# Optimization experiments

Hardware: AMD Instinct MI355X
Metric: run time of the kernel (lower is better)

## Reference

```python
import jax, jax.numpy as jnp
import numpy as np

D = 1024
H = 16
DH = D // H
DFF = 4096
EPS = 1e-5


def new_gelu(u):
    # HF NewGELUActivation: 0.5*u*(1+tanh(sqrt(2/pi)*(u+0.044715*u^3)))
    c = np.sqrt(2.0 / np.pi).astype(np.float32)
    return 0.5 * u * (1.0 + jnp.tanh(c * (u + 0.044715 * u ** 3)))


def layer_norm(u, g, b):
    mu = jnp.mean(u, axis=-1, keepdims=True)
    var = jnp.mean((u - mu) ** 2, axis=-1, keepdims=True)
    return (u - mu) * jax.lax.rsqrt(var + EPS) * g + b


def setup_inputs() -> dict:
    key = jax.random.key(0)
    ks = jax.random.split(key, 12)
    s = 0.02
    inp = {
        "x": jax.random.normal(ks[0], (4, 1024, D), dtype=jnp.float32),
        "Wq": jax.random.normal(ks[1], (D, D), dtype=jnp.float32) * s,
        "bq": jnp.zeros((D,), jnp.float32),
        "Wk": jax.random.normal(ks[2], (D, D), dtype=jnp.float32) * s,
        "bk": jnp.zeros((D,), jnp.float32),
        "Wv": jax.random.normal(ks[3], (D, D), dtype=jnp.float32) * s,
        "bv": jnp.zeros((D,), jnp.float32),
        "Wo": jax.random.normal(ks[4], (D, D), dtype=jnp.float32) * s,
        "bo": jnp.zeros((D,), jnp.float32),
        "g1": jnp.ones((D,), jnp.float32),
        "b1": jnp.zeros((D,), jnp.float32),
        "W1": jax.random.normal(ks[5], (D, DFF), dtype=jnp.float32) * s,
        "bm1": jnp.zeros((DFF,), jnp.float32),
        "W2": jax.random.normal(ks[6], (DFF, D), dtype=jnp.float32) * s,
        "bm2": jnp.zeros((D,), jnp.float32),
        "g2": jnp.ones((D,), jnp.float32),
        "b2": jnp.zeros((D,), jnp.float32),
    }
    return inp


def reference(x, Wq, bq, Wk, bk, Wv, bv, Wo, bo, g1, b1, W1, bm1, W2, bm2, g2, b2):
    B, S, _ = x.shape
    q = (x @ Wq + bq).reshape(B, S, H, DH)
    k = (x @ Wk + bk).reshape(B, S, H, DH)
    v = (x @ Wv + bv).reshape(B, S, H, DH)
    scores = jnp.einsum("bshd,bthd->bhst", q, k) / np.sqrt(DH).astype(np.float32)
    probs = jax.nn.softmax(scores, axis=-1)
    attn = jnp.einsum("bhst,bthd->bshd", probs, v).reshape(B, S, D)
    attn = attn @ Wo + bo
    x1 = layer_norm(x + attn, g1, b1)
    mlp = new_gelu(x1 @ W1 + bm1) @ W2 + bm2
    out = layer_norm(x1 + mlp, g2, b2)
    return out
```

## Files before the change

kernel.cpp:

```cpp
#include <hip/hip_runtime.h>

#define D_    1024
#define HH    16
#define DHEAD 64
#define DFF_  4096
#define NTOK  4096
#define SQLEN 1024

typedef unsigned short ushort_t;
typedef __attribute__((ext_vector_type(8))) short short8;
typedef __attribute__((ext_vector_type(4))) float floatx4;

#define LOG2E 1.44269504f

__device__ __forceinline__ unsigned short f2bf(float f) {
  union { float f; unsigned u; } x; x.f = f;
  unsigned r = x.u + 0x7fffu + ((x.u >> 16) & 1u);
  return (unsigned short)(r >> 16);
}
__device__ __forceinline__ float bf2f(unsigned short u) {
  union { unsigned u; float f; } x; x.u = ((unsigned)u) << 16;
  return x.f;
}
__device__ __forceinline__ unsigned pack2bf_fast(float a, float b) {
  union { float f; unsigned u; } x, y; x.f = a; y.f = b;
  return __builtin_amdgcn_perm(y.u + 0x8000u, x.u + 0x8000u, 0x07060302u);
}
__device__ __forceinline__ float fast_exp2(float x) {
  return __builtin_amdgcn_exp2f(x);
}
__device__ __forceinline__ float fast_gelu(float u) {
  float u2 = u * u;
  float arg = u * (2.30220414f + 0.10294307f * u2);
  float e = __builtin_amdgcn_exp2f(arg);
  float r = __builtin_amdgcn_rcpf(e + 1.0f);
  return u - u * r;
}

__device__ __forceinline__ void async_ld16(const void* g, void* l) {
  __builtin_amdgcn_global_load_lds(
      (const __attribute__((address_space(1))) unsigned int*)g,
      (__attribute__((address_space(3))) unsigned int*)l, 16, 0, 0);
}

__global__ __launch_bounds__(256) void prep_kernel(
    const float* __restrict__ x, const float* __restrict__ Wq,
    const float* __restrict__ Wk, const float* __restrict__ Wv,
    const float* __restrict__ Wo, const float* __restrict__ W1,
    const float* __restrict__ W2,
    ushort_t* __restrict__ xb, ushort_t* __restrict__ wqkvt,
    ushort_t* __restrict__ wot, ushort_t* __restrict__ w1t,
    ushort_t* __restrict__ w2t) {
  int bid = blockIdx.x, tid = threadIdx.x;
  if (bid < 4096) {
    int i = bid * 256 + tid;
    float4 v = ((const float4*)x)[i];
    ushort4 o;
    o.x = f2bf(v.x); o.y = f2bf(v.y); o.z = f2bf(v.z); o.w = f2bf(v.w);
    ((ushort4*)xb)[i] = o;
    return;
  }
  __shared__ float tile[32][33];
  const float* W; ushort_t* T; int K, N, n0, k0;
  if (bid < 8192) {
    int id = bid - 4096, z = id >> 10, xy = id & 1023;
    W = (z == 0) ? Wq : (z == 1) ? Wk : (z == 2) ? Wv : Wo;
    T = (z < 3) ? wqkvt + (size_t)z * D_ * D_ : wot;
    K = D_; N = D_;
    n0 = (xy & 31) * 32; k0 = (xy >> 5) * 32;
  } else if (bid < 12288) {
    int id = bid - 8192;
    W = W1; T = w1t; K = D_; N = DFF_;
    n0 = (id & 127) * 32; k0 = (id >> 7) * 32;
  } else {
    int id = bid - 12288;
    W = W2; T = w2t; K = DFF_; N = D_;
    n0 = (id & 31) * 32; k0 = (id >> 5) * 32;
  }
  int tx = tid & 31, ty = tid >> 5;
#pragma unroll
  for (int i = 0; i < 4; i++)
    tile[ty + i * 8][tx] = W[(size_t)(k0 + ty + i * 8) * N + n0 + tx];
  __syncthreads();
#pragma unroll
  for (int i = 0; i < 4; i++)
    T[(size_t)(n0 + ty + i * 8) * K + k0 + tx] = f2bf(tile[tx][ty + i * 8]);
}

template <int MODE>
__global__ __launch_bounds__(256) void gemm_bf16(
    const ushort_t* __restrict__ A, const ushort_t* __restrict__ Bt,
    int M, int N, int K, int Ks, int nb,
    const float* __restrict__ bias0, const float* __restrict__ bias1,
    const float* __restrict__ bias2,
    ushort_t* __restrict__ o0, ushort_t* __restrict__ o1, ushort_t* __restrict__ o2) {
  __shared__ alignas(16) ushort_t sA[2][128 * 32];
  __shared__ alignas(16) ushort_t sB[2][128 * 32];
  int tid = threadIdx.x;
  int w = tid >> 6, lane = tid & 63, quad = lane >> 4, l16 = lane & 15;
  int wm = w >> 1, wn = w & 1;

  int sp = blockIdx.x / nb;
  int bid = blockIdx.x - sp * nb;
  int gridN = N >> 7;
  int Tn = nb >> 3;
  int lin = (bid & 7) * Tn + (bid >> 3);
  int ng = gridN << 3;
  int gidx = lin / ng;
  int rem = lin - gidx * ng;
  int m0 = ((gidx << 3) + (rem & 7)) << 7;
  int n0 = (rem >> 3) << 7;
  int kbeg = sp * Ks, kend = kbeg + Ks;

  floatx4 acc[4][4];
#pragma unroll
  for (int i = 0; i < 4; i++)
#pragma unroll
    for (int j = 0; j < 4; j++) acc[i][j] = (floatx4){0.f, 0.f, 0.f, 0.f};

  int srow = lane >> 2, scol = (lane & 3) * 8;
  const ushort_t* gA = A + (size_t)(m0 + w * 16 + srow) * K + scol;
  const ushort_t* gB = Bt + (size_t)(n0 + w * 16 + srow) * K + scol;
  ushort_t* lA = sA[0] + w * 16 * 32;
  ushort_t* lB = sB[0] + w * 16 * 32;

  for (int k0 = kbeg; k0 < kend; k0 += 64) {
    __syncthreads();
#pragma unroll
    for (int h = 0; h < 2; h++)
#pragma unroll
      for (int p = 0; p < 2; p++) {
        async_ld16(gA + (size_t)h * 64 * K + k0 + p * 32, lA + p * 4096 + h * 2048);
        async_ld16(gB + (size_t)h * 64 * K + k0 + p * 32, lB + p * 4096 + h * 2048);
      }
    __syncthreads();
#pragma unroll
    for (int kc = 0; kc < 2; kc++) {
      short8 af[4], bfr[4];
#pragma unroll
      for (int mt = 0; mt < 4; mt++)
        af[mt] = *(const short8*)(sA[kc] + (wm * 64 + mt * 16 + l16) * 32 + quad * 8);
#pragma unroll
      for (int nt = 0; nt < 4; nt++)
        bfr[nt] = *(const short8*)(sB[kc] + (wn * 64 + nt * 16 + l16) * 32 + quad * 8);
#pragma unroll
      for (int mt = 0; mt < 4; mt++)
#pragma unroll
        for (int nt = 0; nt < 4; nt++)
          acc[mt][nt] = __builtin_amdgcn_mfma_f32_16x16x32_bf16(af[mt], bfr[nt],
                                                                acc[mt][nt], 0, 0, 0);
    }
  }

  if (MODE == 0) {
#pragma unroll
    for (int nt = 0; nt < 4; nt++) {
      int cg = n0 + wn * 64 + nt * 16 + l16;
      int sel = cg >> 10, nn = cg & 1023;
      const float* bpp = (sel == 0) ? bias0 : ((sel == 1) ? bias1 : bias2);
      float bb = bpp[nn];
      int hh = nn >> 6, dd = nn & 63;
#pragma unroll
      for (int mt = 0; mt < 4; mt++) {
        int rg0 = m0 + wm * 64 + mt * 16 + quad * 4;
        int b0 = rg0 >> 10, s0 = rg0 & 1023;
        if (sel == 2) {
          ushort4 ov;
          ov.x = f2bf(acc[mt][nt][0] + bb);
          ov.y = f2bf(acc[mt][nt][1] + bb);
          ov.z = f2bf(acc[mt][nt][2] + bb);
          ov.w = f2bf(acc[mt][nt][3] + bb);
          *(ushort4*)(o2 + ((size_t)(b0 * HH + hh) * DHEAD + dd) * SQLEN + s0) = ov;
        } else {
          ushort_t* dst = sel ? o1 : o0;
          float sc = (sel == 0) ? (0.125f * LOG2E) : 1.0f;
#pragma unroll
          for (int r = 0; r < 4; r++)
            dst[((size_t)(b0 * HH + hh) * SQLEN + s0 + r) * DHEAD + dd] =
                f2bf((acc[mt][nt][r] + bb) * sc);
        }
      }
    }
  } else {
    size_t rowbase = (size_t)(m0 + wm * 64 + quad * 4) * N + (n0 + wn * 64 + l16);
    if (MODE == 3) rowbase += (size_t)sp * M * N;
    float bb0 = (MODE == 2) ? bias0[(n0 + wn * 64 + l16) & (N - 1)] : 0.f;
    float bb1 = (MODE == 2) ? bias0[(n0 + wn * 64 + 16 + l16) & (N - 1)] : 0.f;
    float bb2 = (MODE == 2) ? bias0[(n0 + wn * 64 + 32 + l16) & (N - 1)] : 0.f;
    float bb3 = (MODE == 2) ? bias0[(n0 + wn * 64 + 48 + l16) & (N - 1)] : 0.f;
#pragma unroll
    for (int mt = 0; mt < 4; mt++) {
#pragma unroll
      for (int r = 0; r < 4; r++) {
        ushort_t* pr = o0 + rowbase + (size_t)(mt * 16 + r) * N;
        if (MODE == 2) {
          pr[0]  = f2bf(fast_gelu(acc[mt][0][r] + bb0));
          pr[16] = f2bf(fast_gelu(acc[mt][1][r] + bb1));
          pr[32] = f2bf(fast_gelu(acc[mt][2][r] + bb2));
          pr[48] = f2bf(fast_gelu(acc[mt][3][r] + bb3));
        } else {
          pr[0]  = f2bf(acc[mt][0][r]);
          pr[16] = f2bf(acc[mt][1][r]);
          pr[32] = f2bf(acc[mt][2][r]);
          pr[48] = f2bf(acc[mt][3][r]);
        }
      }
    }
  }
}

__global__ __launch_bounds__(256) void flash_attn_kernel(const ushort_t* __restrict__ q,
                                                         const ushort_t* __restrict__ k,
                                                         const ushort_t* __restrict__ vt,
                                                         ushort_t* __restrict__ ctx) {
  __shared__ alignas(16) ushort_t sQ[2][128 * 32];
  __shared__ alignas(16) ushort_t sK[2][64 * 32];
  __shared__ alignas(16) ushort_t sVt[2][64 * 32];
  __shared__ alignas(16) char sP[4][2][2][16 * 80];
  int tid = threadIdx.x;
  int w = tid >> 6, lane = tid & 63, quad = lane >> 4, l16 = lane & 15;
  int bh = blockIdx.x, qt = blockIdx.y;
  int b_ = bh >> 4, h_ = bh & 15;

  const ushort_t* Qp = q + ((size_t)bh * SQLEN + qt * 128) * DHEAD;
  const ushort_t* Kp = k + (size_t)bh * SQLEN * DHEAD;
  const ushort_t* Vtp = vt + (size_t)bh * DHEAD * SQLEN;

  int srow = lane >> 2, scol8 = (lane & 3) * 8;

#pragma unroll
  for (int h = 0; h < 2; h++)
#pragma unroll
    for (int p = 0; p < 2; p++)
      async_ld16(Qp + (h * 64 + w * 16 + srow) * 64 + p * 32 + scol8,
                 (char*)sQ + p * 8192 + (h * 64 + w * 16) * 64);

  float l_run[2] = {0.f, 0.f};
  floatx4 o_acc[2][4];
#pragma unroll
  for (int g = 0; g < 2; g++)
#pragma unroll
    for (int dt = 0; dt < 4; dt++) o_acc[g][dt] = (floatx4){0.f, 0.f, 0.f, 0.f};

  for (int kt = 0; kt < 16; kt++) {
    __syncthreads();
#pragma unroll
    for (int t = 0; t < 2; t++) {
      int id = w * 2 + t, panel = id & 1, rg = id >> 1;
      int row = rg * 16 + srow, col = panel * 32 + scol8;
      async_ld16(Kp + kt * 64 * 64 + row * 64 + col,
                 (char*)sK + panel * 4096 + rg * 1024);
      async_ld16(Vtp + (size_t)row * SQLEN + kt * 64 + col,
                 (char*)sVt + panel * 4096 + rg * 1024);
    }
    __syncthreads();

    floatx4 st[2][4];
#pragma unroll
    for (int g = 0; g < 2; g++)
#pragma unroll
      for (int nt = 0; nt < 4; nt++) st[g][nt] = (floatx4){0.f, 0.f, 0.f, 0.f};
#pragma unroll
    for (int kc = 0; kc < 2; kc++) {
      short8 aq0 = *(const short8*)(sQ[kc] + (w * 32 + l16) * 32 + quad * 8);
      short8 aq1 = *(const short8*)(sQ[kc] + (w * 32 + 16 + l16) * 32 + quad * 8);
#pragma unroll
      for (int nt = 0; nt < 4; nt++) {
        short8 kf = *(const short8*)(sK[kc] + (nt * 16 + l16) * 32 + quad * 8);
        st[0][nt] = __builtin_amdgcn_mfma_f32_16x16x32_bf16(kf, aq0, st[0][nt], 0, 0, 0);
        st[1][nt] = __builtin_amdgcn_mfma_f32_16x16x32_bf16(kf, aq1, st[1][nt], 0, 0, 0);
      }
    }

#pragma unroll
    for (int g = 0; g < 2; g++) {
#pragma unroll
      for (int nt = 0; nt < 4; nt++) {
        float p0 = fast_exp2(st[g][nt][0]);
        float p1 = fast_exp2(st[g][nt][1]);
        float p2 = fast_exp2(st[g][nt][2]);
        float p3 = fast_exp2(st[g][nt][3]);
        l_run[g] += (p0 + p1) + (p2 + p3);
        uint2 d2;
        d2.x = pack2bf_fast(p0, p1);
        d2.y = pack2bf_fast(p2, p3);
        *(uint2*)(&sP[w][g][nt >> 1][0] + l16 * 80 + (nt & 1) * 32 + quad * 8) = d2;
      }
    }

#pragma unroll
    for (int kc = 0; kc < 2; kc++) {
      short8 pf0 = *(const short8*)(&sP[w][0][kc][0] + l16 * 80 + quad * 16);
      short8 pf1 = *(const short8*)(&sP[w][1][kc][0] + l16 * 80 + quad * 16);
#pragma unroll
      for (int dt = 0; dt < 4; dt++) {
        short8 vf = *(const short8*)(sVt[kc] + (dt * 16 + l16) * 32 + quad * 8);
        o_acc[0][dt] = __builtin_amdgcn_mfma_f32_16x16x32_bf16(vf, pf0, o_acc[0][dt], 0, 0, 0);
        o_acc[1][dt] = __builtin_amdgcn_mfma_f32_16x16x32_bf16(vf, pf1, o_acc[1][dt], 0, 0, 0);
      }
    }
  }

#pragma unroll
  for (int g = 0; g < 2; g++) {
    float l = l_run[g];
    l += __shfl_xor(l, 16);
    l += __shfl_xor(l, 32);
    float inv = 1.f / fmaxf(l, 1e-30f);
    int s_ = qt * 128 + w * 32 + g * 16 + l16;
    ushort_t* cp = ctx + (size_t)(b_ * SQLEN + s_) * D_ + h_ * DHEAD + quad * 4;
#pragma unroll
    for (int dt = 0; dt < 4; dt++) {
      ushort4 ov;
      ov.x = f2bf(o_acc[g][dt][0] * inv);
      ov.y = f2bf(o_acc[g][dt][1] * inv);
      ov.z = f2bf(o_acc[g][dt][2] * inv);
      ov.w = f2bf(o_acc[g][dt][3] * inv);
      *(ushort4*)(cp + dt * 16) = ov;
    }
  }
}

template <int S, int WB>
__global__ __launch_bounds__(256) void ln_red_kernel(
    const ushort_t* __restrict__ parts, const float* __restrict__ bias,
    const float* __restrict__ res, const float* __restrict__ g,
    const float* __restrict__ b, float* __restrict__ outf,
    ushort_t* __restrict__ outb) {
  int row = blockIdx.x, tid = threadIdx.x;
  float4 v = ((const float4*)(res + (size_t)row * D_))[tid];
  float4 bb = ((const float4*)bias)[tid];
  v.x += bb.x; v.y += bb.y; v.z += bb.z; v.w += bb.w;
#pragma unroll
  for (int s = 0; s < S; s++) {
    ushort4 p = ((const ushort4*)(parts + (size_t)s * NTOK * D_ + (size_t)row * D_))[tid];
    v.x += bf2f(p.x); v.y += bf2f(p.y); v.z += bf2f(p.z); v.w += bf2f(p.w);
  }
  float s1 = v.x + v.y + v.z + v.w;
  float s2 = v.x * v.x + v.y * v.y + v.z * v.z + v.w * v.w;
#pragma unroll
  for (int off = 32; off > 0; off >>= 1) {
    s1 += __shfl_down(s1, off);
    s2 += __shfl_down(s2, off);
  }
  __shared__ float red[10];
  int wid = tid >> 6, lane = tid & 63;
  if (lane == 0) { red[wid] = s1; red[4 + wid] = s2; }
  __syncthreads();
  if (tid == 0) {
    float ts = red[0] + red[1] + red[2] + red[3];
    float ts2 = red[4] + red[5] + red[6] + red[7];
    float mu = ts * (1.f / 1024.f);
    float var = ts2 * (1.f / 1024.f) - mu * mu;
    red[8] = mu;
    red[9] = rsqrtf(var + 1e-5f);
  }
  __syncthreads();
  float mu = red[8], rsg = red[9];
  float4 gv = ((const float4*)g)[tid];
  float4 bv = ((const float4*)b)[tid];
  float4 o;
  o.x = (v.x - mu) * rsg * gv.x + bv.x;
  o.y = (v.y - mu) * rsg * gv.y + bv.y;
  o.z = (v.z - mu) * rsg * gv.z + bv.z;
  o.w = (v.w - mu) * rsg * gv.w + bv.w;
  if (outf) ((float4*)(outf + (size_t)row * D_))[tid] = o;
  if (WB) {
    ushort4 ob;
    ob.x = f2bf(o.x); ob.y = f2bf(o.y); ob.z = f2bf(o.z); ob.w = f2bf(o.w);
    ((ushort4*)(outb + (size_t)row * D_))[tid] = ob;
  }
}

extern "C" void kernel_launch(void* const* d_in, const int* in_sizes, int n_in,
                              void* d_out, int out_size, void* d_ws, size_t ws_size,
                              hipStream_t stream) {
  const float* x   = (const float*)d_in[0];
  const float* Wq  = (const float*)d_in[1];
  const float* bq  = (const float*)d_in[2];
  const float* Wk  = (const float*)d_in[3];
  const float* bk  = (const float*)d_in[4];
  const float* Wv  = (const float*)d_in[5];
  const float* bv  = (const float*)d_in[6];
  const float* Wo  = (const float*)d_in[7];
  const float* bo  = (const float*)d_in[8];
  const float* g1  = (const float*)d_in[9];
  const float* b1  = (const float*)d_in[10];
  const float* W1  = (const float*)d_in[11];
  const float* bm1 = (const float*)d_in[12];
  const float* W2  = (const float*)d_in[13];
  const float* bm2 = (const float*)d_in[14];
  const float* g2  = (const float*)d_in[15];
  const float* b2  = (const float*)d_in[16];
  float* out = (float*)d_out;

  char* ws = (char*)d_ws;
  const size_t MB = 1024 * 1024;
  ushort_t* xb    = (ushort_t*)(ws + 0);
  ushort_t* wqkvt = (ushort_t*)(ws + 8 * MB);
  ushort_t* wot   = (ushort_t*)(ws + 14 * MB);
  ushort_t* w1t   = (ushort_t*)(ws + 16 * MB);
  ushort_t* w2t   = (ushort_t*)(ws + 24 * MB);
  ushort_t* qb    = (ushort_t*)(ws + 32 * MB);
  ushort_t* kb    = (ushort_t*)(ws + 40 * MB);
  ushort_t* vtb   = (ushort_t*)(ws + 48 * MB);
  ushort_t* ctx   = (ushort_t*)(ws + 56 * MB);
  float*    x1    = (float*)   (ws + 64 * MB);
  ushort_t* x1b   = (ushort_t*)(ws + 80 * MB);
  ushort_t* hbuf  = (ushort_t*)(ws + 88 * MB);
  ushort_t* pWo   = (ushort_t*)(ws + 32 * MB);
  ushort_t* pMd   = (ushort_t*)(ws + 32 * MB);
  (void)ws_size; (void)in_sizes; (void)n_in; (void)out_size;

  hipLaunchKernelGGL(prep_kernel, dim3(16384), dim3(256), 0, stream,
                     x, Wq, Wk, Wv, Wo, W1, W2, xb, wqkvt, wot, w1t, w2t);

  hipLaunchKernelGGL((gemm_bf16<0>), dim3(768), dim3(256), 0, stream,
                     xb, wqkvt, NTOK, 3072, D_, D_, 768, bq, bk, bv, qb, kb, vtb);

  hipLaunchKernelGGL(flash_attn_kernel, dim3(4 * HH, SQLEN / 128), dim3(256), 0, stream,
                     qb, kb, vtb, ctx);

  hipLaunchKernelGGL((gemm_bf16<3>), dim3(512), dim3(256), 0, stream,
                     ctx, wot, NTOK, D_, D_, 512, 256,
                     (const float*)nullptr, (const float*)nullptr,
                     (const float*)nullptr, pWo, (ushort_t*)nullptr, (ushort_t*)nullptr);

  hipLaunchKernelGGL((ln_red_kernel<2, 1>), dim3(NTOK), dim3(256), 0, stream,
                     pWo, bo, x, g1, b1, x1, x1b);

  hipLaunchKernelGGL((gemm_bf16<2>), dim3(1024), dim3(256), 0, stream,
                     x1b, w1t, NTOK, DFF_, D_, D_, 1024, bm1, (const float*)nullptr,
                     (const float*)nullptr, hbuf, (ushort_t*)nullptr, (ushort_t*)nullptr);

  hipLaunchKernelGGL((gemm_bf16<3>), dim3(1024), dim3(256), 0, stream,
                     hbuf, w2t, NTOK, D_, DFF_, 1024, 256,
                     (const float*)nullptr, (const float*)nullptr,
                     (const float*)nullptr, pMd, (ushort_t*)nullptr, (ushort_t*)nullptr);

  hipLaunchKernelGGL((ln_red_kernel<4, 0>), dim3(NTOK), dim3(256), 0, stream,
                     pMd, bm2, x1, g2, b2, out, (ushort_t*)nullptr);
}
```

Before: 335.4 us.

## Replace 128x128 GEMM with 256x256 tile, 8-wave, swizzled LDS, pipelined kernel

Replaces the 128x128-tile, 4-wave GEMM with a 256x256-tile, 512-thread kernel. The new kernel uses double-buffered LDS with an XOR swizzle and a four-quadrant software pipeline that interleaves async global-to-LDS loads with MFMA blocks, using explicit waitcnt, barriers and setprio. Split-K factors are changed: the Wo projection now uses 4 splits, so the LN reduction reads 4 partials and the partial buffer moves to a different workspace region. Larger tiles raise data reuse and cut LDS round trips, at the cost of fewer blocks (192-256) on a large GPU and higher register pressure.

```diff
diff --git a/kernel.cpp b/kernel.cpp
--- a/kernel.cpp
+++ b/kernel.cpp
@@ -88,88 +88,145 @@
 }
 
 template <int MODE>
-__global__ __launch_bounds__(256) void gemm_bf16(
+__global__ __launch_bounds__(512, 2) void gemm256(
     const ushort_t* __restrict__ A, const ushort_t* __restrict__ Bt,
     int M, int N, int K, int Ks, int nb,
     const float* __restrict__ bias0, const float* __restrict__ bias1,
     const float* __restrict__ bias2,
     ushort_t* __restrict__ o0, ushort_t* __restrict__ o1, ushort_t* __restrict__ o2) {
-  __shared__ alignas(16) ushort_t sA[2][128 * 32];
-  __shared__ alignas(16) ushort_t sB[2][128 * 32];
+  __shared__ alignas(16) ushort_t sA[2][2][128 * 64];
+  __shared__ alignas(16) ushort_t sB[2][2][128 * 64];
   int tid = threadIdx.x;
   int w = tid >> 6, lane = tid & 63, quad = lane >> 4, l16 = lane & 15;
-  int wm = w >> 1, wn = w & 1;
+  int wm = w >> 2, wn = w & 3;
 
   int sp = blockIdx.x / nb;
   int bid = blockIdx.x - sp * nb;
-  int gridN = N >> 7;
+  int gridN = N >> 8;
   int Tn = nb >> 3;
   int lin = (bid & 7) * Tn + (bid >> 3);
   int ng = gridN << 3;
   int gidx = lin / ng;
   int rem = lin - gidx * ng;
-  int m0 = ((gidx << 3) + (rem & 7)) << 7;
-  int n0 = (rem >> 3) << 7;
-  int kbeg = sp * Ks, kend = kbeg + Ks;
-
-  floatx4 acc[4][4];
-#pragma unroll
-  for (int i = 0; i < 4; i++)
+  int m0 = ((gidx << 3) + (rem & 7)) << 8;
+  int n0 = (rem >> 3) << 8;
+  int kbeg = sp * Ks;
+  int nkt = Ks >> 6;
+
+  floatx4 acc[8][4];
+#pragma unroll
+  for (int i = 0; i < 8; i++)
 #pragma unroll
     for (int j = 0; j < 4; j++) acc[i][j] = (floatx4){0.f, 0.f, 0.f, 0.f};
 
-  int srow = lane >> 2, scol = (lane & 3) * 8;
-  const ushort_t* gA = A + (size_t)(m0 + w * 16 + srow) * K + scol;
-  const ushort_t* gB = Bt + (size_t)(n0 + w * 16 + srow) * K + scol;
-  ushort_t* lA = sA[0] + w * 16 * 32;
-  ushort_t* lB = sB[0] + w * 16 * 32;
-
-  for (int k0 = kbeg; k0 < kend; k0 += 64) {
-    __syncthreads();
-#pragma unroll
-    for (int h = 0; h < 2; h++)
-#pragma unroll
-      for (int p = 0; p < 2; p++) {
-        async_ld16(gA + (size_t)h * 64 * K + k0 + p * 32, lA + p * 4096 + h * 2048);
-        async_ld16(gB + (size_t)h * 64 * K + k0 + p * 32, lB + p * 4096 + h * 2048);
-      }
-    __syncthreads();
-#pragma unroll
-    for (int kc = 0; kc < 2; kc++) {
-      short8 af[4], bfr[4];
-#pragma unroll
-      for (int mt = 0; mt < 4; mt++)
-        af[mt] = *(const short8*)(sA[kc] + (wm * 64 + mt * 16 + l16) * 32 + quad * 8);
-#pragma unroll
-      for (int nt = 0; nt < 4; nt++)
-        bfr[nt] = *(const short8*)(sB[kc] + (wn * 64 + nt * 16 + l16) * 32 + quad * 8);
-#pragma unroll
-      for (int mt = 0; mt < 4; mt++)
-#pragma unroll
-        for (int nt = 0; nt < 4; nt++)
-          acc[mt][nt] = __builtin_amdgcn_mfma_f32_16x16x32_bf16(af[mt], bfr[nt],
-                                                                acc[mt][nt], 0, 0, 0);
-    }
+  int s8  = tid >> 3;
+  int lcx = (tid & 7) ^ (s8 & 7);
+  const ushort_t* gA = A + (size_t)(m0 + s8) * K + kbeg + lcx * 8;
+  const ushort_t* gB = Bt + (size_t)(n0 + (s8 & 31) + (s8 >> 5) * 64) * K + kbeg + lcx * 8;
+  char* sta = (char*)&sA[0][0][0] + w * 1024;
+  char* stb = (char*)&sB[0][0][0] + w * 1024;
+
+  const char* rdA = (const char*)&sA[0][0][0] + (wm * 64 + l16) * 128;
+  const char* rdB = (const char*)&sB[0][0][0] + (wn * 32 + l16) * 128;
+  int kof0 = ((quad ^ (l16 & 7)) << 4);
+  int kof1 = kof0 ^ 64;
+
+#define STG_A(db, h, ko) { const ushort_t* _g = gA + (size_t)(h) * 64 * K + (ko); \
+    char* _l = sta + (db) * 32768 + (h) * 16384; \
+    async_ld16(_g, _l); async_ld16(_g + (size_t)128 * K, _l + 8192); }
+#define STG_B(db, h, ko) { const ushort_t* _g = gB + (size_t)(h) * 32 * K + (ko); \
+    char* _l = stb + (db) * 32768 + (h) * 16384; \
+    async_ld16(_g, _l); async_ld16(_g + (size_t)128 * K, _l + 8192); }
+#define LD_A(db, mq) { const char* _p = rdA + (db) * 32768 + (mq) * 16384; \
+    _Pragma("unroll") for (int mt = 0; mt < 4; mt++) { \
+      a[mt][0] = *(const short8*)(_p + mt * 2048 + kof0); \
+      a[mt][1] = *(const short8*)(_p + mt * 2048 + kof1); } }
+#define LD_B(db, nq) { const char* _p = rdB + (db) * 32768 + (nq) * 16384; \
+    _Pragma("unroll") for (int nt = 0; nt < 2; nt++) { \
+      b[nt][0] = *(const short8*)(_p + nt * 2048 + kof0); \
+      b[nt][1] = *(const short8*)(_p + nt * 2048 + kof1); } }
+#define MFMA_Q(mq, nq) { \
+    _Pragma("unroll") for (int mt = 0; mt < 4; mt++) \
+    _Pragma("unroll") for (int nt = 0; nt < 2; nt++) { \
+      floatx4 c = acc[(mq) * 4 + mt][(nq) * 2 + nt]; \
+      c = __builtin_amdgcn_mfma_f32_16x16x32_bf16(a[mt][0], b[nt][0], c, 0, 0, 0); \
+      c = __builtin_amdgcn_mfma_f32_16x16x32_bf16(a[mt][1], b[nt][1], c, 0, 0, 0); \
+      acc[(mq) * 4 + mt][(nq) * 2 + nt] = c; } }
+#define BAR __builtin_amdgcn_s_barrier()
+#define LGK0 { asm volatile("s_waitcnt lgkmcnt(0)" ::: "memory"); \
+               __builtin_amdgcn_sched_barrier(0); }
+#define VMW4 asm volatile("s_waitcnt vmcnt(4)" ::: "memory")
+#define VMW2 asm volatile("s_waitcnt vmcnt(2)" ::: "memory")
+#define VMW0 asm volatile("s_waitcnt vmcnt(0)" ::: "memory")
+#define PRIO1 __builtin_amdgcn_s_setprio(1)
+#define PRIO0 __builtin_amdgcn_s_setprio(0)
+
+  short8 a[4][2], b[2][2];
+
+  STG_A(0, 0, 0); STG_B(0, 0, 0); STG_B(0, 1, 0); STG_A(0, 1, 0);
+  VMW4; BAR;
+
+  for (int kt = 0; kt + 1 < nkt; kt++) {
+    int db = kt & 1, dn = db ^ 1;
+    int ko = (kt + 1) << 6;
+    LD_A(db, 0); LD_B(db, 0);
+    STG_A(dn, 0, ko);
+    BAR; LGK0;
+    PRIO1; MFMA_Q(0, 0); PRIO0;
+    VMW4; BAR;
+    LD_B(db, 1);
+    STG_B(dn, 0, ko);
+    BAR; LGK0;
+    PRIO1; MFMA_Q(0, 1); PRIO0;
+    VMW4; BAR;
+    LD_A(db, 1);
+    STG_B(dn, 1, ko);
+    BAR; LGK0;
+    PRIO1; MFMA_Q(1, 1); PRIO0;
+    BAR;
+    LD_B(db, 0);
+    STG_A(dn, 1, ko);
+    BAR; LGK0;
+    PRIO1; MFMA_Q(1, 0); PRIO0;
+    VMW4; BAR;
+  }
+  {
+    int db = (nkt - 1) & 1;
+    LD_A(db, 0); LD_B(db, 0);
+    BAR; LGK0;
+    PRIO1; MFMA_Q(0, 0); PRIO0;
+    VMW2; BAR;
+    LD_B(db, 1);
+    BAR; LGK0;
+    PRIO1; MFMA_Q(0, 1); PRIO0;
+    VMW0; BAR;
+    LD_A(db, 1);
+    BAR; LGK0;
+    PRIO1; MFMA_Q(1, 1); PRIO0;
+    BAR;
+    LD_B(db, 0);
+    BAR; LGK0;
+    PRIO1; MFMA_Q(1, 0); PRIO0;
   }
 
   if (MODE == 0) {
 #pragma unroll
-    for (int nt = 0; nt < 4; nt++) {
-      int cg = n0 + wn * 64 + nt * 16 + l16;
+    for (int bj = 0; bj < 4; bj++) {
+      int cg = n0 + wn * 64 + (bj >> 1) * 32 + (bj & 1) * 16 + l16;
       int sel = cg >> 10, nn = cg & 1023;
       const float* bpp = (sel == 0) ? bias0 : ((sel == 1) ? bias1 : bias2);
       float bb = bpp[nn];
       int hh = nn >> 6, dd = nn & 63;
 #pragma unroll
-      for (int mt = 0; mt < 4; mt++) {
-        int rg0 = m0 + wm * 64 + mt * 16 + quad * 4;
+      for (int ai = 0; ai < 8; ai++) {
+        int rg0 = m0 + wm * 128 + (ai >> 2) * 64 + (ai & 3) * 16 + quad * 4;
         int b0 = rg0 >> 10, s0 = rg0 & 1023;
         if (sel == 2) {
           ushort4 ov;
-          ov.x = f2bf(acc[mt][nt][0] + bb);
-          ov.y = f2bf(acc[mt][nt][1] + bb);
-          ov.z = f2bf(acc[mt][nt][2] + bb);
-          ov.w = f2bf(acc[mt][nt][3] + bb);
+          ov.x = f2bf(acc[ai][bj][0] + bb);
+          ov.y = f2bf(acc[ai][bj][1] + bb);
+          ov.z = f2bf(acc[ai][bj][2] + bb);
+          ov.w = f2bf(acc[ai][bj][3] + bb);
           *(ushort4*)(o2 + ((size_t)(b0 * HH + hh) * DHEAD + dd) * SQLEN + s0) = ov;
         } else {
           ushort_t* dst = sel ? o1 : o0;
@@ -177,36 +234,50 @@
 #pragma unroll
           for (int r = 0; r < 4; r++)
             dst[((size_t)(b0 * HH + hh) * SQLEN + s0 + r) * DHEAD + dd] =
-                f2bf((acc[mt][nt][r] + bb) * sc);
+                f2bf((acc[ai][bj][r] + bb) * sc);
         }
       }
     }
   } else {
-    size_t rowbase = (size_t)(m0 + wm * 64 + quad * 4) * N + (n0 + wn * 64 + l16);
+    size_t rowbase = (size_t)(m0 + wm * 128 + quad * 4) * N + (n0 + wn * 64 + l16);
     if (MODE == 3) rowbase += (size_t)sp * M * N;
-    float bb0 = (MODE == 2) ? bias0[(n0 + wn * 64 + l16) & (N - 1)] : 0.f;
-    float bb1 = (MODE == 2) ? bias0[(n0 + wn * 64 + 16 + l16) & (N - 1)] : 0.f;
-    float bb2 = (MODE == 2) ? bias0[(n0 + wn * 64 + 32 + l16) & (N - 1)] : 0.f;
-    float bb3 = (MODE == 2) ? bias0[(n0 + wn * 64 + 48 + l16) & (N - 1)] : 0.f;
-#pragma unroll
-    for (int mt = 0; mt < 4; mt++) {
+    float bb[4];
+    if (MODE == 2) {
+#pragma unroll
+      for (int c = 0; c < 4; c++)
+        bb[c] = bias0[(n0 + wn * 64 + c * 16 + l16) & (N - 1)];
+    }
+#pragma unroll
+    for (int ai = 0; ai < 8; ai++) {
 #pragma unroll
       for (int r = 0; r < 4; r++) {
-        ushort_t* pr = o0 + rowbase + (size_t)(mt * 16 + r) * N;
+        ushort_t* pr = o0 + rowbase + (size_t)((ai >> 2) * 64 + (ai & 3) * 16 + r) * N;
         if (MODE == 2) {
-          pr[0]  = f2bf(fast_gelu(acc[mt][0][r] + bb0));
-          pr[16] = f2bf(fast_gelu(acc[mt][1][r] + bb1));
-          pr[32] = f2bf(fast_gelu(acc[mt][2][r] + bb2));
-          pr[48] = f2bf(fast_gelu(acc[mt][3][r] + bb3));
+          pr[0]  = f2bf(fast_gelu(acc[ai][0][r] + bb[0]));
+          pr[16] = f2bf(fast_gelu(acc[ai][1][r] + bb[1]));
+          pr[32] = f2bf(fast_gelu(acc[ai][2][r] + bb[2]));
+          pr[48] = f2bf(fast_gelu(acc[ai][3][r] + bb[3]));
         } else {
-          pr[0]  = f2bf(acc[mt][0][r]);
-          pr[16] = f2bf(acc[mt][1][r]);
-          pr[32] = f2bf(acc[mt][2][r]);
-          pr[48] = f2bf(acc[mt][3][r]);
+          pr[0]  = f2bf(acc[ai][0][r]);
+          pr[16] = f2bf(acc[ai][1][r]);
+          pr[32] = f2bf(acc[ai][2][r]);
+          pr[48] = f2bf(acc[ai][3][r]);
         }
       }
     }
   }
+#undef STG_A
+#undef STG_B
+#undef LD_A
+#undef LD_B
+#undef MFMA_Q
+#undef BAR
+#undef LGK0
+#undef VMW4
+#undef VMW2
+#undef VMW0
+#undef PRIO1
+#undef PRIO0
 }
 
 __global__ __launch_bounds__(256) void flash_attn_kernel(const ushort_t* __restrict__ q,
@@ -408,33 +479,33 @@
   float*    x1    = (float*)   (ws + 64 * MB);
   ushort_t* x1b   = (ushort_t*)(ws + 80 * MB);
   ushort_t* hbuf  = (ushort_t*)(ws + 88 * MB);
-  ushort_t* pWo   = (ushort_t*)(ws + 32 * MB);
+  ushort_t* pWo   = (ushort_t*)(ws + 88 * MB);
   ushort_t* pMd   = (ushort_t*)(ws + 32 * MB);
   (void)ws_size; (void)in_sizes; (void)n_in; (void)out_size;
 
   hipLaunchKernelGGL(prep_kernel, dim3(16384), dim3(256), 0, stream,
                      x, Wq, Wk, Wv, Wo, W1, W2, xb, wqkvt, wot, w1t, w2t);
 
-  hipLaunchKernelGGL((gemm_bf16<0>), dim3(768), dim3(256), 0, stream,
-                     xb, wqkvt, NTOK, 3072, D_, D_, 768, bq, bk, bv, qb, kb, vtb);
+  hipLaunchKernelGGL((gemm256<0>), dim3(192), dim3(512), 0, stream,
+                     xb, wqkvt, NTOK, 3072, D_, 1024, 192, bq, bk, bv, qb, kb, vtb);
 
   hipLaunchKernelGGL(flash_attn_kernel, dim3(4 * HH, SQLEN / 128), dim3(256), 0, stream,
                      qb, kb, vtb, ctx);
 
-  hipLaunchKernelGGL((gemm_bf16<3>), dim3(512), dim3(256), 0, stream,
-                     ctx, wot, NTOK, D_, D_, 512, 256,
+  hipLaunchKernelGGL((gemm256<3>), dim3(256), dim3(512), 0, stream,
+                     ctx, wot, NTOK, D_, D_, 256, 64,
                      (const float*)nullptr, (const float*)nullptr,
                      (const float*)nullptr, pWo, (ushort_t*)nullptr, (ushort_t*)nullptr);
 
-  hipLaunchKernelGGL((ln_red_kernel<2, 1>), dim3(NTOK), dim3(256), 0, stream,
+  hipLaunchKernelGGL((ln_red_kernel<4, 1>), dim3(NTOK), dim3(256), 0, stream,
                      pWo, bo, x, g1, b1, x1, x1b);
 
-  hipLaunchKernelGGL((gemm_bf16<2>), dim3(1024), dim3(256), 0, stream,
-                     x1b, w1t, NTOK, DFF_, D_, D_, 1024, bm1, (const float*)nullptr,
+  hipLaunchKernelGGL((gemm256<2>), dim3(256), dim3(512), 0, stream,
+                     x1b, w1t, NTOK, DFF_, D_, 1024, 256, bm1, (const float*)nullptr,
                      (const float*)nullptr, hbuf, (ushort_t*)nullptr, (ushort_t*)nullptr);
 
-  hipLaunchKernelGGL((gemm_bf16<3>), dim3(1024), dim3(256), 0, stream,
-                     hbuf, w2t, NTOK, D_, DFF_, 1024, 256,
+  hipLaunchKernelGGL((gemm256<3>), dim3(256), dim3(512), 0, stream,
+                     hbuf, w2t, NTOK, D_, DFF_, 1024, 64,
                      (const float*)nullptr, (const float*)nullptr,
                      (const float*)nullptr, pMd, (ushort_t*)nullptr, (ushort_t*)nullptr);
 
```

New measurement: 326.5 us. 1.03x faster.
